# Performance work log

Measured on AMD Instinct MI355X. Metric: run time of the kernel, lower is better.

The kernel has to match this reference:

```python
import jax, jax.numpy as jnp
import numpy as np

POOLED = 7          # output_size
SCALE = 0.25        # spatial_scale
SRATIO = 2          # sampling_ratio (fixed in module)
IMG_H, IMG_W = 800.0, 1216.0


def setup_inputs() -> dict:
    key = jax.random.key(0)
    kf, kb, kx, ky, kw, kh = jax.random.split(key, 6)
    B, C, H, W = 2, 256, 200, 304
    features = jax.random.normal(kf, (B, C, H, W), dtype=jnp.float32)
    N = 1000
    bidx = jax.random.randint(kb, (N,), 0, B).astype(jnp.float32)
    x1 = jax.random.uniform(kx, (N,), minval=0.0, maxval=IMG_W - 32.0)
    y1 = jax.random.uniform(ky, (N,), minval=0.0, maxval=IMG_H - 32.0)
    bw = jax.random.uniform(kw, (N,), minval=16.0, maxval=256.0)
    bh = jax.random.uniform(kh, (N,), minval=16.0, maxval=256.0)
    x2 = jnp.minimum(x1 + bw, IMG_W)
    y2 = jnp.minimum(y1 + bh, IMG_H)
    rois = jnp.stack([bidx, x1, y1, x2, y2], axis=1).astype(jnp.float32)
    return {"features": features, "rois": rois}


def _axis_interp(c, size):
    """Per-axis bilinear prep, matching torchvision roi_align (aligned=False)."""
    valid = (c >= -1.0) & (c <= size)
    c = jnp.maximum(c, 0.0)
    lo = jnp.floor(c).astype(jnp.int32)
    at_edge = lo >= size - 1
    lo = jnp.minimum(lo, size - 1)
    hi = jnp.minimum(lo + 1, size - 1)
    c = jnp.where(at_edge, lo.astype(c.dtype), c)
    frac = c - lo.astype(c.dtype)
    return lo, hi, frac, valid


def reference(features, rois):
    B, C, H, W = features.shape
    N = rois.shape[0]
    P, s = POOLED, SRATIO
    Ps = P * s

    f = jnp.transpose(features, (0, 2, 3, 1))  # [B, H, W, C]
    b = rois[:, 0].astype(jnp.int32)
    x1 = rois[:, 1] * SCALE
    y1 = rois[:, 2] * SCALE
    x2 = rois[:, 3] * SCALE
    y2 = rois[:, 4] * SCALE
    roi_w = jnp.maximum(x2 - x1, 1.0)
    roi_h = jnp.maximum(y2 - y1, 1.0)
    bin_w = roi_w / P
    bin_h = roi_h / P

    # sample-point centers: ph*bin + (iy+0.5)*bin/s  ==  (idx+0.5)/s * bin
    off = (jnp.arange(Ps, dtype=jnp.float32) + 0.5) / s  # [Ps]
    ys = y1[:, None] + off[None, :] * bin_h[:, None]     # [N, Ps]
    xs = x1[:, None] + off[None, :] * bin_w[:, None]     # [N, Ps]

    yl, yh, ly, vy = _axis_interp(ys, H)
    xl, xh, lx, vx = _axis_interp(xs, W)
    hy, hx = 1.0 - ly, 1.0 - lx

    bb = b[:, None, None]
    YL, YH = yl[:, :, None], yh[:, :, None]
    XL, XH = xl[:, None, :], xh[:, None, :]
    # gathered corner values: [N, Ps, Ps, C]
    v11 = f[bb, YL, XL]
    v12 = f[bb, YL, XH]
    v21 = f[bb, YH, XL]
    v22 = f[bb, YH, XH]

    w11 = (hy[:, :, None] * hx[:, None, :])[..., None]
    w12 = (hy[:, :, None] * lx[:, None, :])[..., None]
    w21 = (ly[:, :, None] * hx[:, None, :])[..., None]
    w22 = (ly[:, :, None] * lx[:, None, :])[..., None]
    mask = (vy[:, :, None] & vx[:, None, :]).astype(f.dtype)[..., None]

    val = (w11 * v11 + w12 * v12 + w21 * v21 + w22 * v22) * mask  # [N,Ps,Ps,C]
    out = val.reshape(N, P, s, P, s, C).mean(axis=(2, 4))          # [N,P,P,C]
    return jnp.transpose(out, (0, 3, 1, 2))                        # [N,C,P,P]
```

## Files before the change

kernel.cpp:

```cpp
#include <hip/hip_runtime.h>
#include <hip/hip_fp16.h>

#define POOLED 7
#define PP 49
#define ROI_SCALE 0.25f
#define FH 200
#define FW 304
#define FHW 60800
#define FC 256
#define RS 271

__global__ __launch_bounds__(256) void transpose_f16(
    const float* __restrict__ in, __half* __restrict__ out)
{
    __shared__ float tile[64][33];
    const int b   = blockIdx.z;
    const int hw0 = blockIdx.x * 32;
    const int c0  = blockIdx.y * 64;
    const int tx  = threadIdx.x;
    const int ty  = threadIdx.y;

    #pragma unroll
    for (int i = 0; i < 8; i++) {
        int c = c0 + ty + i * 8;
        tile[ty + i * 8][tx] = in[((size_t)b * FC + c) * FHW + hw0 + tx];
    }
    __syncthreads();
    #pragma unroll
    for (int i = 0; i < 4; i++) {
        int hwl = ty + i * 8;
        __half2 h = __floats2half2_rn(tile[2 * tx][hwl], tile[2 * tx + 1][hwl]);
        *reinterpret_cast<__half2*>(
            out + ((size_t)b * FHW + hwl + hw0) * FC + c0 + 2 * tx) = h;
    }
}

__device__ __forceinline__ void ld8(const __half* p, float o[8]) {
    uint4 u = *reinterpret_cast<const uint4*>(p);
    const __half2* h = reinterpret_cast<const __half2*>(&u);
    #pragma unroll
    for (int j = 0; j < 4; j++) {
        float2 f = __half22float2(h[j]);
        o[2 * j]     = f.x;
        o[2 * j + 1] = f.y;
    }
}

__global__ __launch_bounds__(512) void roi_gather_f16(
    const __half* __restrict__ f,
    const float* __restrict__ rois,
    float* __restrict__ out)
{
    __shared__ float s_out[PP * RS];

    const int n    = blockIdx.x;
    const int tid  = threadIdx.x;
    const int wave = tid >> 6;
    const int lane = tid & 63;
    const int hl   = lane & 31;
    const bool hiHalf = lane >= 32;

    const float* r = rois + (size_t)n * 5;
    const int   bi = (int)r[0];
    const float x1 = r[1] * ROI_SCALE;
    const float y1 = r[2] * ROI_SCALE;
    const float bin_w = fmaxf(r[3] * ROI_SCALE - x1, 1.0f) / (float)POOLED;
    const float bin_h = fmaxf(r[4] * ROI_SCALE - y1, 1.0f) / (float)POOLED;

    const __half* base = f + (size_t)bi * (FHW * FC) + 8 * hl;
    const int c0  = 8 * hl;
    const int swz = 2 * (hl >> 2);

    #pragma unroll 2
    for (int bin = wave; bin < PP; bin += 8) {
        const int ph = bin / 7;
        const int pw = bin - ph * 7;

        int rowlo[2], rowhi[2];
        float why[2], wly[2];
        #pragma unroll
        for (int iy = 0; iy < 2; iy++) {
            float c = y1 + ((float)(2 * ph + iy) + 0.5f) * 0.5f * bin_h;
            float v = ((c >= -1.0f) && (c <= (float)FH)) ? 1.0f : 0.0f;
            c = fmaxf(c, 0.0f);
            int lo = (int)floorf(c);
            bool edge = (lo >= FH - 1);
            lo = min(lo, FH - 1);
            rowlo[iy] = lo * FW;
            rowhi[iy] = min(lo + 1, FH - 1) * FW;
            float ly = edge ? 0.0f : (c - (float)lo);
            why[iy] = v * (1.0f - ly);
            wly[iy] = v * ly;
        }
        int   xoff[2];
        float wx[2];
        #pragma unroll
        for (int ix = 0; ix < 2; ix++) {
            float c = x1 + ((float)(2 * pw + ix) + 0.5f) * 0.5f * bin_w;
            float v = ((c >= -1.0f) && (c <= (float)FW)) ? 1.0f : 0.0f;
            c = fmaxf(c, 0.0f);
            int lo = (int)floorf(c);
            bool edge = (lo >= FW - 1);
            lo = min(lo, FW - 1);
            int hi = min(lo + 1, FW - 1);
            float lx = edge ? 0.0f : (c - (float)lo);
            xoff[ix] = hiHalf ? hi : lo;
            wx[ix]   = v * (hiHalf ? lx : (1.0f - lx));
        }

        float acc[8] = {0.f, 0.f, 0.f, 0.f, 0.f, 0.f, 0.f, 0.f};
        #pragma unroll
        for (int iy = 0; iy < 2; iy++) {
            #pragma unroll
            for (int ix = 0; ix < 2; ix++) {
                float vlo[8], vhi[8];
                ld8(base + ((rowlo[iy] + xoff[ix]) << 8), vlo);
                ld8(base + ((rowhi[iy] + xoff[ix]) << 8), vhi);
                float wlo = why[iy] * wx[ix];
                float whi = wly[iy] * wx[ix];
                #pragma unroll
                for (int k = 0; k < 8; k++)
                    acc[k] += wlo * vlo[k] + whi * vhi[k];
            }
        }

        #pragma unroll
        for (int k = 0; k < 8; k++)
            acc[k] += __shfl_xor(acc[k], 32, 64);

        if (!hiHalf) {
            float* so = s_out + bin * RS + c0 + swz;
            #pragma unroll
            for (int k = 0; k < 8; k++)
                so[k] = acc[k] * 0.25f;
        }
    }
    __syncthreads();

    float* ob = out + (size_t)n * (FC * PP);
    for (int i = tid; i < FC * PP; i += 512) {
        int c = i / PP;
        int b = i - c * PP;
        ob[i] = s_out[b * RS + c + 2 * (c >> 5)];
    }
}

__global__ __launch_bounds__(256) void roi_align_fallback(
    const float* __restrict__ feat,
    const float* __restrict__ rois,
    float* __restrict__ out,
    int C, int H, int W, int N)
{
    int idx = blockIdx.x * blockDim.x + threadIdx.x;
    int total = N * C * PP;
    if (idx >= total) return;

    int pw = idx % POOLED;
    int ph = (idx / POOLED) % POOLED;
    int c  = (idx / PP) % C;
    int n  = idx / (PP * C);

    const float* r = rois + (size_t)n * 5;
    int   b  = (int)r[0];
    float x1 = r[1] * ROI_SCALE;
    float y1 = r[2] * ROI_SCALE;
    float bin_w = fmaxf(r[3] * ROI_SCALE - x1, 1.0f) / (float)POOLED;
    float bin_h = fmaxf(r[4] * ROI_SCALE - y1, 1.0f) / (float)POOLED;

    const float* fc = feat + ((size_t)b * C + c) * (size_t)(H * W);

    float acc = 0.0f;
    #pragma unroll
    for (int iy = 0; iy < 2; iy++) {
        float yy = y1 + ((float)(ph * 2 + iy) + 0.5f) * bin_h * 0.5f;
        bool  vy = (yy >= -1.0f) && (yy <= (float)H);
        float cy = fmaxf(yy, 0.0f);
        int   ylo = (int)floorf(cy);
        bool  ey = (ylo >= H - 1);
        ylo = min(ylo, H - 1);
        int   yhi = min(ylo + 1, H - 1);
        if (ey) cy = (float)ylo;
        float ly = cy - (float)ylo, hy = 1.0f - ly;

        #pragma unroll
        for (int ix = 0; ix < 2; ix++) {
            float xx = x1 + ((float)(pw * 2 + ix) + 0.5f) * bin_w * 0.5f;
            bool  vx = (xx >= -1.0f) && (xx <= (float)W);
            float cx = fmaxf(xx, 0.0f);
            int   xlo = (int)floorf(cx);
            bool  ex = (xlo >= W - 1);
            xlo = min(xlo, W - 1);
            int   xhi = min(xlo + 1, W - 1);
            if (ex) cx = (float)xlo;
            float lx = cx - (float)xlo, hx = 1.0f - lx;

            if (vy && vx) {
                float v11 = fc[(size_t)ylo * W + xlo];
                float v12 = fc[(size_t)ylo * W + xhi];
                float v21 = fc[(size_t)yhi * W + xlo];
                float v22 = fc[(size_t)yhi * W + xhi];
                acc += hy * (hx * v11 + lx * v12) + ly * (hx * v21 + lx * v22);
            }
        }
    }
    out[idx] = acc * 0.25f;
}

extern "C" void kernel_launch(void* const* d_in, const int* in_sizes, int n_in,
                              void* d_out, int out_size, void* d_ws, size_t ws_size,
                              hipStream_t stream) {
    const float* feat = (const float*)d_in[0];
    const float* rois = (const float*)d_in[1];
    float* out = (float*)d_out;

    const int N = in_sizes[1] / 5;
    const int B = in_sizes[0] / (FC * FHW);

    size_t need = (size_t)B * FHW * FC * sizeof(__half);
    if (ws_size >= need) {
        __half* f16 = (__half*)d_ws;
        transpose_f16<<<dim3(FHW / 32, FC / 64, B), dim3(32, 8), 0, stream>>>(feat, f16);
        roi_gather_f16<<<N, 512, 0, stream>>>(f16, rois, out);
    } else {
        int total = N * FC * PP;
        roi_align_fallback<<<(total + 255) / 256, 256, 0, stream>>>(feat, rois, out, FC, FH, FW, N);
    }
}
```

Before: 80.28 us.

## Sort ROIs by Morton order and map to XCDs for L2 locality

Adds a single-block bitonic sort kernel that orders ROIs by batch index and a Morton code of their center. The gather kernel then remaps block IDs so that each XCD, taking blocks round-robin, processes a contiguous run of spatially nearby ROIs, with the aim of reusing overlapping feature rows in that XCD's L2. It also issues all eight corner loads before any conversion to raise memory-level parallelism, and sets an occupancy hint in launch_bounds. The extra sort launch adds a small serial cost.

```diff
diff --git a/kernel.cpp b/kernel.cpp
--- a/kernel.cpp
+++ b/kernel.cpp
@@ -10,6 +10,42 @@
 #define FC 256
 #define RS 271
 
+__global__ __launch_bounds__(1024) void sort_rois(
+    const float* __restrict__ rois, int N, unsigned* __restrict__ perm)
+{
+    __shared__ unsigned key[1024];
+    const int t = threadIdx.x;
+    unsigned v = 0xFFFFFFFFu;
+    if (t < N) {
+        const float* r = rois + (size_t)t * 5;
+        int b = (int)r[0];
+        float yc = (r[2] + r[4]) * (0.5f * ROI_SCALE);
+        float xc = (r[1] + r[3]) * (0.5f * ROI_SCALE);
+        int yq = min(127, max(0, (int)yc >> 1));
+        int xq = min(127, max(0, (int)xc >> 2));
+        unsigned m = 0;
+        #pragma unroll
+        for (int i = 0; i < 7; i++)
+            m |= (((unsigned)((yq >> i) & 1)) << (2 * i + 1)) |
+                 (((unsigned)((xq >> i) & 1)) << (2 * i));
+        v = ((unsigned)b << 25) | (m << 10) | (unsigned)t;
+    }
+    key[t] = v;
+    __syncthreads();
+    for (int k = 2; k <= 1024; k <<= 1) {
+        for (int j = k >> 1; j > 0; j >>= 1) {
+            int p = t ^ j;
+            if (p > t) {
+                unsigned a = key[t], b2 = key[p];
+                bool sw = ((t & k) == 0) ? (a > b2) : (a < b2);
+                if (sw) { key[t] = b2; key[p] = a; }
+            }
+            __syncthreads();
+        }
+    }
+    if (t < N) perm[t] = key[t];
+}
+
 __global__ __launch_bounds__(256) void transpose_f16(
     const float* __restrict__ in, __half* __restrict__ out)
 {
@@ -35,25 +71,27 @@
     }
 }
 
-__device__ __forceinline__ void ld8(const __half* p, float o[8]) {
-    uint4 u = *reinterpret_cast<const uint4*>(p);
-    const __half2* h = reinterpret_cast<const __half2*>(&u);
-    #pragma unroll
-    for (int j = 0; j < 4; j++) {
-        float2 f = __half22float2(h[j]);
-        o[2 * j]     = f.x;
-        o[2 * j + 1] = f.y;
-    }
-}
-
-__global__ __launch_bounds__(512) void roi_gather_f16(
+__global__ __launch_bounds__(512, 6) void roi_gather_f16(
     const __half* __restrict__ f,
     const float* __restrict__ rois,
-    float* __restrict__ out)
+    const unsigned* __restrict__ perm,
+    float* __restrict__ out,
+    int N, int useperm)
 {
     __shared__ float s_out[PP * RS];
 
-    const int n    = blockIdx.x;
+    const int bid = blockIdx.x;
+    int n;
+    if (useperm) {
+        int xcd = bid & 7, pos = bid >> 3;
+        int q = N >> 3, rr = N & 7;
+        int sidx = (xcd < rr) ? xcd * (q + 1) + pos
+                              : rr * (q + 1) + (xcd - rr) * q + pos;
+        n = (int)(perm[sidx] & 1023u);
+    } else {
+        n = bid;
+    }
+
     const int tid  = threadIdx.x;
     const int wave = tid >> 6;
     const int lane = tid & 63;
@@ -71,7 +109,6 @@
     const int c0  = 8 * hl;
     const int swz = 2 * (hl >> 2);
 
-    #pragma unroll 2
     for (int bin = wave; bin < PP; bin += 8) {
         const int ph = bin / 7;
         const int pw = bin - ph * 7;
@@ -108,19 +145,29 @@
             wx[ix]   = v * (hiHalf ? lx : (1.0f - lx));
         }
 
+        uint4 u[8];
+        #pragma unroll
+        for (int s = 0; s < 4; s++) {
+            int iy = s >> 1, ix = s & 1;
+            int px = xoff[ix];
+            u[2 * s]     = *reinterpret_cast<const uint4*>(base + ((rowlo[iy] + px) << 8));
+            u[2 * s + 1] = *reinterpret_cast<const uint4*>(base + ((rowhi[iy] + px) << 8));
+        }
+
         float acc[8] = {0.f, 0.f, 0.f, 0.f, 0.f, 0.f, 0.f, 0.f};
         #pragma unroll
-        for (int iy = 0; iy < 2; iy++) {
+        for (int s = 0; s < 4; s++) {
+            int iy = s >> 1, ix = s & 1;
+            float wlo = why[iy] * wx[ix];
+            float whi = wly[iy] * wx[ix];
+            const __half2* hlo = reinterpret_cast<const __half2*>(&u[2 * s]);
+            const __half2* hhi = reinterpret_cast<const __half2*>(&u[2 * s + 1]);
             #pragma unroll
-            for (int ix = 0; ix < 2; ix++) {
-                float vlo[8], vhi[8];
-                ld8(base + ((rowlo[iy] + xoff[ix]) << 8), vlo);
-                ld8(base + ((rowhi[iy] + xoff[ix]) << 8), vhi);
-                float wlo = why[iy] * wx[ix];
-                float whi = wly[iy] * wx[ix];
-                #pragma unroll
-                for (int k = 0; k < 8; k++)
-                    acc[k] += wlo * vlo[k] + whi * vhi[k];
+            for (int j = 0; j < 4; j++) {
+                float2 flo = __half22float2(hlo[j]);
+                float2 fhi = __half22float2(hhi[j]);
+                acc[2 * j]     += wlo * flo.x + whi * fhi.x;
+                acc[2 * j + 1] += wlo * flo.y + whi * fhi.y;
             }
         }
 
@@ -216,11 +263,18 @@
     const int N = in_sizes[1] / 5;
     const int B = in_sizes[0] / (FC * FHW);
 
-    size_t need = (size_t)B * FHW * FC * sizeof(__half);
+    const size_t featBytes = (size_t)B * FHW * FC * sizeof(__half);
+    const size_t permOff   = (featBytes + 255) & ~(size_t)255;
+    const size_t need      = permOff + 1024 * sizeof(unsigned);
+
     if (ws_size >= need) {
-        __half* f16 = (__half*)d_ws;
+        __half*   f16  = (__half*)d_ws;
+        unsigned* perm = (unsigned*)((char*)d_ws + permOff);
+        int useperm = (N <= 1024) ? 1 : 0;
+        if (useperm)
+            sort_rois<<<1, 1024, 0, stream>>>(rois, N, perm);
         transpose_f16<<<dim3(FHW / 32, FC / 64, B), dim3(32, 8), 0, stream>>>(feat, f16);
-        roi_gather_f16<<<N, 512, 0, stream>>>(f16, rois, out);
+        roi_gather_f16<<<N, 512, 0, stream>>>(f16, rois, perm, out, N, useperm);
     } else {
         int total = N * FC * PP;
         roi_align_fallback<<<(total + 255) / 256, 256, 0, stream>>>(feat, rois, out, FC, FH, FW, N);
```

Result: no change. 79.58 us (-0.9%).

## Batch two bins' gathers per wave, shrink staging to fp16, raise occupancy hint

Applied to the files above, without the earlier changes.

Each wave now issues all 16 corner loads for two bins before doing any FMAs, so more memory requests are in flight per wave. The shared-memory staging buffer changes from fp32 to fp16 with vectorized 16-byte stores, which roughly halves LDS use. The launch bounds now ask for 8 blocks per CU. The trade-off is more registers per thread and an extra rounding of the pooled outputs to fp16, which costs some accuracy.

```diff
diff --git a/kernel.cpp b/kernel.cpp
--- a/kernel.cpp
+++ b/kernel.cpp
@@ -8,7 +8,7 @@
 #define FW 304
 #define FHW 60800
 #define FC 256
-#define RS 271
+#define SR 264
 
 __global__ __launch_bounds__(256) void transpose_f16(
     const float* __restrict__ in, __half* __restrict__ out)
@@ -35,23 +35,97 @@
     }
 }
 
-__device__ __forceinline__ void ld8(const __half* p, float o[8]) {
-    uint4 u = *reinterpret_cast<const uint4*>(p);
-    const __half2* h = reinterpret_cast<const __half2*>(&u);
-    #pragma unroll
-    for (int j = 0; j < 4; j++) {
-        float2 f = __half22float2(h[j]);
-        o[2 * j]     = f.x;
-        o[2 * j + 1] = f.y;
-    }
-}
-
-__global__ __launch_bounds__(512) void roi_gather_f16(
+struct Bin {
+    int   row[2][2];
+    int   xo[2];
+    float wy[2][2];
+    float wx[2];
+};
+
+__device__ __forceinline__ void mkbin(int bin, float x1, float y1,
+                                      float bin_w, float bin_h, bool hiHalf, Bin& p)
+{
+    const int ph = bin / 7;
+    const int pw = bin - ph * 7;
+    #pragma unroll
+    for (int iy = 0; iy < 2; iy++) {
+        float c = y1 + ((float)(2 * ph + iy) + 0.5f) * 0.5f * bin_h;
+        float v = ((c >= -1.0f) && (c <= (float)FH)) ? 1.0f : 0.0f;
+        c = fmaxf(c, 0.0f);
+        int lo = (int)floorf(c);
+        bool edge = (lo >= FH - 1);
+        lo = min(lo, FH - 1);
+        p.row[iy][0] = lo * FW;
+        p.row[iy][1] = min(lo + 1, FH - 1) * FW;
+        float ly = edge ? 0.0f : (c - (float)lo);
+        p.wy[iy][0] = v * (1.0f - ly);
+        p.wy[iy][1] = v * ly;
+    }
+    #pragma unroll
+    for (int ix = 0; ix < 2; ix++) {
+        float c = x1 + ((float)(2 * pw + ix) + 0.5f) * 0.5f * bin_w;
+        float v = ((c >= -1.0f) && (c <= (float)FW)) ? 1.0f : 0.0f;
+        c = fmaxf(c, 0.0f);
+        int lo = (int)floorf(c);
+        bool edge = (lo >= FW - 1);
+        lo = min(lo, FW - 1);
+        int hi = min(lo + 1, FW - 1);
+        float lx = edge ? 0.0f : (c - (float)lo);
+        p.xo[ix] = hiHalf ? hi : lo;
+        p.wx[ix] = v * (hiHalf ? lx : (1.0f - lx));
+    }
+}
+
+__device__ __forceinline__ void ldbin(const __half* base, const Bin& p, uint4* u)
+{
+    #pragma unroll
+    for (int s = 0; s < 4; s++) {
+        int iy = s >> 1, ix = s & 1;
+        u[2 * s]     = *reinterpret_cast<const uint4*>(base + ((p.row[iy][0] + p.xo[ix]) << 8));
+        u[2 * s + 1] = *reinterpret_cast<const uint4*>(base + ((p.row[iy][1] + p.xo[ix]) << 8));
+    }
+}
+
+__device__ __forceinline__ void fmabin(const Bin& p, const uint4* u, float* acc)
+{
+    #pragma unroll
+    for (int s = 0; s < 4; s++) {
+        int iy = s >> 1, ix = s & 1;
+        float wlo = p.wy[iy][0] * p.wx[ix];
+        float whi = p.wy[iy][1] * p.wx[ix];
+        const __half2* hlo = reinterpret_cast<const __half2*>(&u[2 * s]);
+        const __half2* hhi = reinterpret_cast<const __half2*>(&u[2 * s + 1]);
+        #pragma unroll
+        for (int j = 0; j < 4; j++) {
+            float2 flo = __half22float2(hlo[j]);
+            float2 fhi = __half22float2(hhi[j]);
+            acc[2 * j]     += wlo * flo.x + whi * fhi.x;
+            acc[2 * j + 1] += wlo * flo.y + whi * fhi.y;
+        }
+    }
+}
+
+__device__ __forceinline__ void finbin(int bin, int c0, bool hiHalf,
+                                       float* acc, __half* s_h)
+{
+    #pragma unroll
+    for (int k = 0; k < 8; k++)
+        acc[k] += __shfl_xor(acc[k], 32, 64);
+    if (!hiHalf) {
+        union { __half2 h2[4]; uint4 u; } cv;
+        #pragma unroll
+        for (int j = 0; j < 4; j++)
+            cv.h2[j] = __floats2half2_rn(acc[2 * j] * 0.25f, acc[2 * j + 1] * 0.25f);
+        *reinterpret_cast<uint4*>(s_h + bin * SR + c0) = cv.u;
+    }
+}
+
+__global__ __launch_bounds__(512, 8) void roi_gather_f16(
     const __half* __restrict__ f,
     const float* __restrict__ rois,
     float* __restrict__ out)
 {
-    __shared__ float s_out[PP * RS];
+    __shared__ __half s_h[PP * SR];
 
     const int n    = blockIdx.x;
     const int tid  = threadIdx.x;
@@ -68,72 +142,37 @@
     const float bin_h = fmaxf(r[4] * ROI_SCALE - y1, 1.0f) / (float)POOLED;
 
     const __half* base = f + (size_t)bi * (FHW * FC) + 8 * hl;
-    const int c0  = 8 * hl;
-    const int swz = 2 * (hl >> 2);
-
-    #pragma unroll 2
-    for (int bin = wave; bin < PP; bin += 8) {
-        const int ph = bin / 7;
-        const int pw = bin - ph * 7;
-
-        int rowlo[2], rowhi[2];
-        float why[2], wly[2];
-        #pragma unroll
-        for (int iy = 0; iy < 2; iy++) {
-            float c = y1 + ((float)(2 * ph + iy) + 0.5f) * 0.5f * bin_h;
-            float v = ((c >= -1.0f) && (c <= (float)FH)) ? 1.0f : 0.0f;
-            c = fmaxf(c, 0.0f);
-            int lo = (int)floorf(c);
-            bool edge = (lo >= FH - 1);
-            lo = min(lo, FH - 1);
-            rowlo[iy] = lo * FW;
-            rowhi[iy] = min(lo + 1, FH - 1) * FW;
-            float ly = edge ? 0.0f : (c - (float)lo);
-            why[iy] = v * (1.0f - ly);
-            wly[iy] = v * ly;
-        }
-        int   xoff[2];
-        float wx[2];
-        #pragma unroll
-        for (int ix = 0; ix < 2; ix++) {
-            float c = x1 + ((float)(2 * pw + ix) + 0.5f) * 0.5f * bin_w;
-            float v = ((c >= -1.0f) && (c <= (float)FW)) ? 1.0f : 0.0f;
-            c = fmaxf(c, 0.0f);
-            int lo = (int)floorf(c);
-            bool edge = (lo >= FW - 1);
-            lo = min(lo, FW - 1);
-            int hi = min(lo + 1, FW - 1);
-            float lx = edge ? 0.0f : (c - (float)lo);
-            xoff[ix] = hiHalf ? hi : lo;
-            wx[ix]   = v * (hiHalf ? lx : (1.0f - lx));
-        }
-
+    const int c0 = 8 * hl;
+
+    #pragma unroll
+    for (int pr = 0; pr < 3; pr++) {
+        const int binA = wave + 16 * pr;
+        const int binB = binA + 8;
+
+        Bin pA, pB;
+        mkbin(binA, x1, y1, bin_w, bin_h, hiHalf, pA);
+        mkbin(binB, x1, y1, bin_w, bin_h, hiHalf, pB);
+
+        uint4 u[16];
+        ldbin(base, pA, u);
+        ldbin(base, pB, u + 8);
+
+        float accA[8] = {0.f, 0.f, 0.f, 0.f, 0.f, 0.f, 0.f, 0.f};
+        float accB[8] = {0.f, 0.f, 0.f, 0.f, 0.f, 0.f, 0.f, 0.f};
+        fmabin(pA, u, accA);
+        fmabin(pB, u + 8, accB);
+
+        finbin(binA, c0, hiHalf, accA, s_h);
+        finbin(binB, c0, hiHalf, accB, s_h);
+    }
+    if (wave == 0) {
+        Bin p;
+        mkbin(48, x1, y1, bin_w, bin_h, hiHalf, p);
+        uint4 u[8];
+        ldbin(base, p, u);
         float acc[8] = {0.f, 0.f, 0.f, 0.f, 0.f, 0.f, 0.f, 0.f};
-        #pragma unroll
-        for (int iy = 0; iy < 2; iy++) {
-            #pragma unroll
-            for (int ix = 0; ix < 2; ix++) {
-                float vlo[8], vhi[8];
-                ld8(base + ((rowlo[iy] + xoff[ix]) << 8), vlo);
-                ld8(base + ((rowhi[iy] + xoff[ix]) << 8), vhi);
-                float wlo = why[iy] * wx[ix];
-                float whi = wly[iy] * wx[ix];
-                #pragma unroll
-                for (int k = 0; k < 8; k++)
-                    acc[k] += wlo * vlo[k] + whi * vhi[k];
-            }
-        }
-
-        #pragma unroll
-        for (int k = 0; k < 8; k++)
-            acc[k] += __shfl_xor(acc[k], 32, 64);
-
-        if (!hiHalf) {
-            float* so = s_out + bin * RS + c0 + swz;
-            #pragma unroll
-            for (int k = 0; k < 8; k++)
-                so[k] = acc[k] * 0.25f;
-        }
+        fmabin(p, u, acc);
+        finbin(48, c0, hiHalf, acc, s_h);
     }
     __syncthreads();
 
@@ -141,7 +180,7 @@
     for (int i = tid; i < FC * PP; i += 512) {
         int c = i / PP;
         int b = i - c * PP;
-        ob[i] = s_out[b * RS + c + 2 * (c >> 5)];
+        ob[i] = __half2float(s_h[b * SR + c]);
     }
 }
 
@@ -216,7 +255,7 @@
     const int N = in_sizes[1] / 5;
     const int B = in_sizes[0] / (FC * FHW);
 
-    size_t need = (size_t)B * FHW * FC * sizeof(__half);
+    const size_t need = (size_t)B * FHW * FC * sizeof(__half);
     if (ws_size >= need) {
         __half* f16 = (__half*)d_ws;
         transpose_f16<<<dim3(FHW / 32, FC / 64, B), dim3(32, 8), 0, stream>>>(feat, f16);
```

Result: slower. 126.4 us (+57.4%).
